# Optimization experiments

Hardware: AMD Instinct MI355X
Metric: run time of the kernel (lower is better)

Reference implementation:

```python
import jax, jax.numpy as jnp
import numpy as np

H = 8
D_MODEL = 512
D_K = D_MODEL // H
B = 8
S = 1024


def _linear(x, W, b):
    # torch nn.Linear: y = x @ W.T + b, W: [out, in]
    return jnp.einsum('bsd,ed->bse', x, W) + b


def _to_heads(x):
    # [B,S,D] -> [B,H,S,d_k]
    return x.reshape(B, S, H, D_K).transpose(0, 2, 1, 3)


def setup_inputs() -> dict:
    key = jax.random.key(0)
    ks = jax.random.split(key, 20)
    inp = {
        'input_rgb': jax.random.normal(ks[0], (B, S, D_MODEL), jnp.float32),
        'input_flow': jax.random.normal(ks[1], (B, S, D_MODEL), jnp.float32),
    }
    names = ['Wq1', 'Wk1', 'Wv1', 'Wq2', 'Wk2', 'Wv2', 'Wo1', 'Wo2']
    for i, n in enumerate(names):
        inp[n] = jax.random.normal(ks[2 + i], (D_MODEL, D_MODEL), jnp.float32) * 0.02
        inp['b' + n[1:]] = jax.random.normal(ks[10 + i], (D_MODEL,), jnp.float32) * 0.02
    return inp


def reference(input_rgb, input_flow, Wq1, bq1, Wk1, bk1, Wv1, bv1,
              Wq2, bq2, Wk2, bk2, Wv2, bv2, Wo1, bo1, Wo2, bo2):
    scale = 1.0 / jnp.sqrt(jnp.asarray(D_K, input_rgb.dtype))

    q_r = _to_heads(_linear(input_rgb, Wq1, bq1))
    k_r = _to_heads(_linear(input_rgb, Wk1, bk1))
    v_r = _to_heads(_linear(input_rgb, Wv1, bv1))
    q_f = _to_heads(_linear(input_flow, Wq2, bq2))
    k_f = _to_heads(_linear(input_flow, Wk2, bk2))
    v_f = _to_heads(_linear(input_flow, Wv2, bv2))

    # two full [B,H,S,S] softmax attention maps
    attn_rgb = jax.nn.softmax(jnp.einsum('bhqd,bhkd->bhqk', q_r, k_r) * scale, axis=-1)
    attn_flow = jax.nn.softmax(jnp.einsum('bhqd,bhkd->bhqk', q_f, k_f) * scale, axis=-1)
    # elementwise max merge (breaks flash-attention fusion)
    attn = jnp.maximum(attn_rgb, attn_flow)

    # Attention2: out = attn @ value (dropout is identity in eval mode)
    out_rgb = jnp.einsum('bhqk,bhkd->bhqd', attn, v_r)
    out_flow = jnp.einsum('bhqk,bhkd->bhqd', attn, v_f)

    out_rgb = out_rgb.transpose(0, 2, 1, 3).reshape(B, S, D_MODEL)
    out_flow = out_flow.transpose(0, 2, 1, 3).reshape(B, S, D_MODEL)
    return (_linear(out_rgb, Wo1, bo1), _linear(out_flow, Wo2, bo2))
```

## Files before the change

### kernel.cpp

```cpp
#include <hip/hip_runtime.h>
#include <hip/hip_bf16.h>


typedef unsigned short u16;
typedef __attribute__((ext_vector_type(8))) short short8;
typedef __attribute__((ext_vector_type(4))) short s4pack;
typedef __attribute__((ext_vector_type(4))) float floatx4;

#define B_DIM 8
#define S_DIM 1024
#define H_DIM 8
#define DK 64
#define DMODEL 512
#define NTOK (B_DIM * S_DIM)
#define SEG ((size_t)NTOK * DMODEL)
#define WSEG ((size_t)DMODEL * DMODEL)

#define SCHED_FENCE() __builtin_amdgcn_sched_barrier(0)
#define LGKM0() asm volatile("s_waitcnt lgkmcnt(0)" ::: "memory")
#define VMCNT0() asm volatile("s_waitcnt vmcnt(0)" ::: "memory")
#define BARRIER() __builtin_amdgcn_s_barrier()

__device__ __forceinline__ floatx4 mfma_bf16(short8 a, short8 b, floatx4 c) {
  return __builtin_amdgcn_mfma_f32_16x16x32_bf16(a, b, c, 0, 0, 0);
}

__device__ __forceinline__ u16 f32_to_bf16_rne(float f) {
  unsigned u = __float_as_uint(f);
  unsigned r = u + 0x7FFFu + ((u >> 16) & 1u);
  return (u16)(r >> 16);
}

__device__ __forceinline__ float bf16_bits_to_f32(u16 u) {
  return __uint_as_float(((unsigned)u) << 16);
}

__device__ __forceinline__ void async_cp16(const u16* g, u16* lds) {
  __builtin_amdgcn_global_load_lds(
      (__attribute__((address_space(1))) void*)(const_cast<u16*>(g)),
      (__attribute__((address_space(3))) void*)(lds), 16, 0, 0);
}

#define NT_CONV 18
struct ConvParams {
  const void* src[NT_CONV];
  u16* dst[NT_CONV];
  int n[NT_CONV];
  int coff[NT_CONV + 1];
};

__global__ __launch_bounds__(256) void convert_inputs(ConvParams p) {
  __shared__ int flag_f32;
  const int blk = blockIdx.x;
  int t = 0;
  while (t + 1 < NT_CONV && blk >= p.coff[t + 1]) ++t;
  const int lc = blk - p.coff[t];
  const int n = p.n[t];
  const int tid = threadIdx.x;

  if (tid < 64) {
    const u16* s = (const u16*)p.src[t];
    int bad = 0;
#pragma unroll
    for (int j = 0; j < 8; ++j) {
      float f = bf16_bits_to_f32(s[tid * 8 + j]);
      bad |= !(fabsf(f) < 1e4f);
    }
    bad |= __shfl_xor(bad, 1);
    bad |= __shfl_xor(bad, 2);
    bad |= __shfl_xor(bad, 4);
    bad |= __shfl_xor(bad, 8);
    bad |= __shfl_xor(bad, 16);
    bad |= __shfl_xor(bad, 32);
    if (tid == 0) flag_f32 = bad;
  }
  __syncthreads();
  const int is_f32 = flag_f32;
  const int base = lc * 65536;

  for (int it = 0; it < 32; ++it) {
    const int idx = base + (it * 256 + tid) * 8;
    if (idx + 8 > n) break;
    if (!is_f32) {
      *(short8*)&p.dst[t][idx] = *(const short8*)&((const u16*)p.src[t])[idx];
    } else {
      const float* s = (const float*)p.src[t] + idx;
      short8 o;
#pragma unroll
      for (int j = 0; j < 8; ++j) o[j] = (short)f32_to_bf16_rne(s[j]);
      *(short8*)&p.dst[t][idx] = o;
    }
  }
}

__device__ __forceinline__ void gemm128_mainloop(
    const u16* __restrict__ A, const u16* __restrict__ W,
    int m0, int n0, int K, u16* ldsA, u16* ldsB, floatx4 acc[4][4]) {
  const int tid = threadIdx.x;
  const int lane = tid & 63;
  const int wid = tid >> 6;
  const int wm = wid >> 1, wn = wid & 1;
  const int r = lane & 15, g = lane >> 4;

  const int stg_row = wid * 32 + (lane >> 2);
  const int stg_col = (lane & 3) * 8;

  const u16* ga0 = A + (size_t)(m0 + stg_row) * K + stg_col;
  const u16* ga1 = A + (size_t)(m0 + stg_row + 16) * K + stg_col;
  const u16* gb0 = W + (size_t)(n0 + stg_row) * K + stg_col;
  const u16* gb1 = W + (size_t)(n0 + stg_row + 16) * K + stg_col;
  const int lo0 = (wid * 32) * 32;
  const int lo1 = (wid * 32 + 16) * 32;

  async_cp16(ga0, ldsA + lo0);
  async_cp16(ga1, ldsA + lo1);
  async_cp16(gb0, ldsB + lo0);
  async_cp16(gb1, ldsB + lo1);
  VMCNT0();
  BARRIER();

  int cur = 0;
  for (int k0 = 0; k0 < K; k0 += 32) {
    const int nxt = cur ^ 1;
    const bool more = (k0 + 32 < K);
    if (more) {
      const int nb = nxt * 4096;
      async_cp16(ga0 + k0 + 32, ldsA + nb + lo0);
      async_cp16(ga1 + k0 + 32, ldsA + nb + lo1);
      async_cp16(gb0 + k0 + 32, ldsB + nb + lo0);
      async_cp16(gb1 + k0 + 32, ldsB + nb + lo1);
    }
    const int cb = cur * 4096;
    short8 a[4], b[4];
#pragma unroll
    for (int i = 0; i < 4; ++i)
      a[i] = *(const short8*)&ldsA[cb + (wm * 64 + i * 16 + r) * 32 + g * 8];
#pragma unroll
    for (int j = 0; j < 4; ++j)
      b[j] = *(const short8*)&ldsB[cb + (wn * 64 + j * 16 + r) * 32 + g * 8];
#pragma unroll
    for (int i = 0; i < 4; ++i)
#pragma unroll
      for (int j = 0; j < 4; ++j)
        acc[i][j] = mfma_bf16(a[i], b[j], acc[i][j]);
    if (more) {
      SCHED_FENCE(); VMCNT0(); BARRIER(); SCHED_FENCE();
      cur = nxt;
    }
  }
}

struct QkvParams {
  const u16* X[2];
  const u16* W[2][3];
  const u16* Bias[2][3];
  u16* Out[2][3];
};

__global__ __launch_bounds__(256) void qkv_gemm(QkvParams p) {
  __shared__ u16 ldsA[2 * 128 * 32];
  __shared__ u16 ldsB[2 * 128 * 32];
  const int z = blockIdx.z;
  const int wi = blockIdx.y >> 2;
  const int n0 = (blockIdx.y & 3) * 128;
  const int m0 = blockIdx.x * 128;

  floatx4 acc[4][4];
  const floatx4 z4 = {0.f, 0.f, 0.f, 0.f};
#pragma unroll
  for (int i = 0; i < 4; ++i)
#pragma unroll
    for (int j = 0; j < 4; ++j) acc[i][j] = z4;

  gemm128_mainloop(p.X[z], p.W[z][wi], m0, n0, DMODEL, ldsA, ldsB, acc);

  const int tid = threadIdx.x, lane = tid & 63, wid = tid >> 6;
  const int wm = wid >> 1, wn = wid & 1, r = lane & 15, g = lane >> 4;
  const u16* bias = p.Bias[z][wi];
  u16* out = p.Out[z][wi];
  const float qscale = 0.125f * 1.4426950408889634f;

#pragma unroll
  for (int j = 0; j < 4; ++j) {
    const int c = n0 + wn * 64 + j * 16 + r;
    const float bv = bf16_bits_to_f32(bias[c]);
    const int h = c >> 6, d = c & 63;
#pragma unroll
    for (int i = 0; i < 4; ++i) {
      const int row0 = m0 + wm * 64 + i * 16 + g * 4;
      const int bb = row0 >> 10, ss0 = row0 & 1023;
      if (wi == 2) {
        s4pack pk;
#pragma unroll
        for (int ii = 0; ii < 4; ++ii)
          pk[ii] = (short)f32_to_bf16_rne(acc[i][j][ii] + bv);
        *(s4pack*)&out[(((size_t)(bb * H_DIM + h)) * DK + d) * S_DIM + ss0] = pk;
      } else {
#pragma unroll
        for (int ii = 0; ii < 4; ++ii) {
          float v = acc[i][j][ii] + bv;
          if (wi == 0) v *= qscale;
          out[(((size_t)(bb * H_DIM + h)) * S_DIM + (ss0 + ii)) * DK + d] =
              f32_to_bf16_rne(v);
        }
      }
    }
  }
}

#define KVB 32
#define QB 64

struct AttnParams {
  const u16* Q[2];
  const u16* K[2];
  const u16* Vt[2];
  u16* O[2];
};

__global__ __launch_bounds__(256, 4) void attn_merged(AttnParams p) {
  __shared__ u16 Ks[2][KVB * 64];
  __shared__ u16 Vs[2][64 * KVB];
  __shared__ u16 Ps[QB * 40];

  const int tid = threadIdx.x;
  const int lane = tid & 63;
  const int wid = tid >> 6;
  const int r = lane & 15, g = lane >> 4;

  const int lin = blockIdx.x;
  const int w = (lin & 7) * 128 + (lin >> 3);
  const int bh = w >> 4;
  const int q0 = (w & 15) * QB;
  const size_t hbase = (size_t)bh * S_DIM * DK;

  const int krow = tid >> 3, kch = tid & 7;
  const int kdst = krow * 64 + ((kch ^ (krow & 7)) * 8);
  const size_t kgsrc = (size_t)krow * DK + kch * 8;
  const int vrow = tid >> 2, vch = tid & 3;
  const int vdst = vrow * KVB + ((vch ^ ((vrow >> 2) & 3)) * 8);
  const size_t vgsrc = (size_t)vrow * S_DIM + vch * 8;

  short8 qf[2][2];
#pragma unroll
  for (int s = 0; s < 2; ++s)
#pragma unroll
    for (int kc = 0; kc < 2; ++kc)
      qf[s][kc] = *(const short8*)
          &p.Q[s][hbase + (size_t)(q0 + wid * 16 + r) * DK + kc * 32 + g * 8];

  short8 kst[2], vst[2];
#pragma unroll
  for (int s = 0; s < 2; ++s)
    kst[s] = *(const short8*)&p.K[s][hbase + kgsrc];

  float sums[2][4];
#pragma unroll
  for (int s = 0; s < 2; ++s)
#pragma unroll
    for (int i = 0; i < 4; ++i) sums[s][i] = 0.f;

  for (int kt = 0; kt < 32; ++kt) {
    if (kt) { SCHED_FENCE(); BARRIER(); SCHED_FENCE(); }
#pragma unroll
    for (int s = 0; s < 2; ++s)
      *(short8*)&Ks[s][kdst] = kst[s];
    if (kt < 31) {
      const size_t k0n = (size_t)(kt + 1) * KVB * DK;
#pragma unroll
      for (int s = 0; s < 2; ++s)
        kst[s] = *(const short8*)&p.K[s][hbase + k0n + kgsrc];
    }
    SCHED_FENCE(); LGKM0(); BARRIER(); SCHED_FENCE();

#pragma unroll
    for (int s = 0; s < 2; ++s)
#pragma unroll
      for (int nt = 0; nt < 2; ++nt) {
        const int row = nt * 16 + r;
        const short8 b0 = *(const short8*)&Ks[s][row * 64 + ((g ^ (r & 7)) * 8)];
        const short8 b1 =
            *(const short8*)&Ks[s][row * 64 + (((4 + g) ^ (r & 7)) * 8)];
        floatx4 acc = {0.f, 0.f, 0.f, 0.f};
        acc = mfma_bf16(qf[s][0], b0, acc);
        acc = mfma_bf16(qf[s][1], b1, acc);
#pragma unroll
        for (int i = 0; i < 4; ++i)
          sums[s][i] += __builtin_amdgcn_exp2f(acc[i]);
      }
  }

#pragma unroll
  for (int s = 0; s < 2; ++s) {
    kst[s] = *(const short8*)&p.K[s][hbase + kgsrc];
    vst[s] = *(const short8*)&p.Vt[s][hbase + vgsrc];
  }

  float inv_[2][4];
#pragma unroll
  for (int s = 0; s < 2; ++s)
#pragma unroll
    for (int i = 0; i < 4; ++i) {
      float v = sums[s][i];
      v += __shfl_xor(v, 1);
      v += __shfl_xor(v, 2);
      v += __shfl_xor(v, 4);
      v += __shfl_xor(v, 8);
      inv_[s][i] = 1.0f / v;
    }

  floatx4 o_[2][4];
  const floatx4 z4 = {0.f, 0.f, 0.f, 0.f};
#pragma unroll
  for (int s = 0; s < 2; ++s)
#pragma unroll
    for (int nt = 0; nt < 4; ++nt) o_[s][nt] = z4;

  for (int kt = 0; kt < 32; ++kt) {
    SCHED_FENCE(); BARRIER(); SCHED_FENCE();
#pragma unroll
    for (int s = 0; s < 2; ++s) {
      *(short8*)&Ks[s][kdst] = kst[s];
      *(short8*)&Vs[s][vdst] = vst[s];
    }
    if (kt < 31) {
      const size_t kn = (size_t)(kt + 1) * KVB;
#pragma unroll
      for (int s = 0; s < 2; ++s) {
        kst[s] = *(const short8*)&p.K[s][hbase + kn * DK + kgsrc];
        vst[s] = *(const short8*)&p.Vt[s][hbase + vgsrc + kn];
      }
    }
    SCHED_FENCE(); LGKM0(); BARRIER(); SCHED_FENCE();

#pragma unroll
    for (int nt = 0; nt < 2; ++nt) {
      const int row = nt * 16 + r;
      const short8 br0 = *(const short8*)&Ks[0][row * 64 + ((g ^ (r & 7)) * 8)];
      const short8 br1 =
          *(const short8*)&Ks[0][row * 64 + (((4 + g) ^ (r & 7)) * 8)];
      const short8 bf0 = *(const short8*)&Ks[1][row * 64 + ((g ^ (r & 7)) * 8)];
      const short8 bf1 =
          *(const short8*)&Ks[1][row * 64 + (((4 + g) ^ (r & 7)) * 8)];
      floatx4 ar = {0.f, 0.f, 0.f, 0.f};
      floatx4 af = {0.f, 0.f, 0.f, 0.f};
      ar = mfma_bf16(qf[0][0], br0, ar);
      ar = mfma_bf16(qf[0][1], br1, ar);
      af = mfma_bf16(qf[1][0], bf0, af);
      af = mfma_bf16(qf[1][1], bf1, af);
      const int prow = wid * 16 + g * 4;
#pragma unroll
      for (int i = 0; i < 4; ++i) {
        const float pr = __builtin_amdgcn_exp2f(ar[i]) * inv_[0][i];
        const float pf = __builtin_amdgcn_exp2f(af[i]) * inv_[1][i];
        Ps[(prow + i) * 40 + nt * 16 + r] = f32_to_bf16_rne(fmaxf(pr, pf));
      }
    }

    LGKM0();
    SCHED_FENCE();

    const short8 pa = *(const short8*)&Ps[(wid * 16 + r) * 40 + g * 8];
#pragma unroll
    for (int s = 0; s < 2; ++s)
#pragma unroll
      for (int nt = 0; nt < 4; ++nt) {
        const int vr = nt * 16 + r;
        const short8 v = *(const short8*)
            &Vs[s][vr * KVB + ((g ^ ((r >> 2) & 3)) * 8)];
        o_[s][nt] = mfma_bf16(pa, v, o_[s][nt]);
      }
  }

  const int bb = bh >> 3, h = bh & 7;
#pragma unroll
  for (int s = 0; s < 2; ++s) {
    u16* out = p.O[s];
#pragma unroll
    for (int nt = 0; nt < 4; ++nt) {
      const int col = h * 64 + nt * 16 + r;
#pragma unroll
      for (int i = 0; i < 4; ++i) {
        const int row = q0 + wid * 16 + g * 4 + i;
        out[((size_t)bb * S_DIM + row) * DMODEL + col] =
            f32_to_bf16_rne(o_[s][nt][i]);
      }
    }
  }
}

struct OutParams {
  const u16* A[2];
  const u16* W[2];
  const u16* Bias[2];
  float* Out[2];
};

__global__ __launch_bounds__(256) void out_gemm(OutParams p) {
  __shared__ u16 ldsA[2 * 128 * 32];
  __shared__ u16 ldsB[2 * 128 * 32];
  const int z = blockIdx.z;
  const int m0 = blockIdx.x * 128;
  const int n0 = blockIdx.y * 128;

  floatx4 acc[4][4];
  const floatx4 z4 = {0.f, 0.f, 0.f, 0.f};
#pragma unroll
  for (int i = 0; i < 4; ++i)
#pragma unroll
    for (int j = 0; j < 4; ++j) acc[i][j] = z4;

  gemm128_mainloop(p.A[z], p.W[z], m0, n0, DMODEL, ldsA, ldsB, acc);

  const int tid = threadIdx.x, lane = tid & 63, wid = tid >> 6;
  const int wm = wid >> 1, wn = wid & 1, r = lane & 15, g = lane >> 4;
  const u16* bias = p.Bias[z];
  float* out = p.Out[z];

#pragma unroll
  for (int j = 0; j < 4; ++j) {
    const int c = n0 + wn * 64 + j * 16 + r;
    const float bv = bf16_bits_to_f32(bias[c]);
#pragma unroll
    for (int i = 0; i < 4; ++i) {
      const int row0 = m0 + wm * 64 + i * 16 + g * 4;
#pragma unroll
      for (int ii = 0; ii < 4; ++ii)
        out[(size_t)(row0 + ii) * DMODEL + c] = acc[i][j][ii] + bv;
    }
  }
}

extern "C" void kernel_launch(void* const* d_in, const int* in_sizes, int n_in,
                              void* d_out, int out_size, void* d_ws, size_t ws_size,
                              hipStream_t stream) {
  (void)in_sizes; (void)n_in; (void)out_size; (void)ws_size;
  u16* ws = (u16*)d_ws;
  u16* Qr = ws + 0 * SEG;
  u16* Kr = ws + 1 * SEG;
  u16* Vr = ws + 2 * SEG;
  u16* Qf = ws + 3 * SEG;
  u16* Kf = ws + 4 * SEG;
  u16* Vf = ws + 5 * SEG;
  u16* Or = ws + 6 * SEG;
  u16* Of = ws + 7 * SEG;
  u16* cW = ws + 8 * SEG;
  u16* cB = cW + 8 * WSEG;

  ConvParams cp;
  int coff = 0;
  for (int i = 0; i < NT_CONV; ++i) {
    cp.src[i] = d_in[i];
    int n;
    if (i < 2) {
      n = (int)SEG;
      cp.dst[i] = (i == 0) ? Or : Of;
    } else {
      const int k = (i - 2) >> 1;
      const int isb = (i - 2) & 1;
      n = isb ? DMODEL : (int)WSEG;
      cp.dst[i] = isb ? (cB + k * DMODEL) : (cW + k * WSEG);
    }
    cp.n[i] = n;
    cp.coff[i] = coff;
    coff += (n + 65535) / 65536;
  }
  cp.coff[NT_CONV] = coff;
  convert_inputs<<<dim3(coff), dim3(256), 0, stream>>>(cp);

  QkvParams qp;
  qp.X[0] = Or;
  qp.X[1] = Of;
  for (int s = 0; s < 2; ++s)
    for (int wi = 0; wi < 3; ++wi) {
      const int k = s * 3 + wi;
      qp.W[s][wi] = cW + k * WSEG;
      qp.Bias[s][wi] = cB + k * DMODEL;
    }
  qp.Out[0][0] = Qr; qp.Out[0][1] = Kr; qp.Out[0][2] = Vr;
  qp.Out[1][0] = Qf; qp.Out[1][1] = Kf; qp.Out[1][2] = Vf;
  qkv_gemm<<<dim3(64, 12, 2), dim3(256), 0, stream>>>(qp);

  AttnParams ap;
  ap.Q[0] = Qr; ap.Q[1] = Qf;
  ap.K[0] = Kr; ap.K[1] = Kf;
  ap.Vt[0] = Vr; ap.Vt[1] = Vf;
  ap.O[0] = Or; ap.O[1] = Of;
  attn_merged<<<dim3(1024), dim3(256), 0, stream>>>(ap);

  OutParams op;
  op.A[0] = Or; op.A[1] = Of;
  op.W[0] = cW + 6 * WSEG; op.Bias[0] = cB + 6 * DMODEL;
  op.W[1] = cW + 7 * WSEG; op.Bias[1] = cB + 7 * DMODEL;
  op.Out[0] = (float*)d_out;
  op.Out[1] = (float*)d_out + SEG;
  out_gemm<<<dim3(64, 4, 2), dim3(256), 0, stream>>>(op);
}
```

Measured before the change: 280.7 us.

## Triple-buffer GEMM loads, remap GEMM blocks, keep attention P in registers

```diff
diff --git a/kernel.cpp b/kernel.cpp
--- a/kernel.cpp
+++ b/kernel.cpp
@@ -25,6 +25,11 @@
   return __builtin_amdgcn_mfma_f32_16x16x32_bf16(a, b, c, 0, 0, 0);
 }
 
+__device__ __forceinline__ void mfma16(floatx4& c, s4pack a, s4pack b) {
+  asm volatile("v_mfma_f32_16x16x16_bf16 %0, %1, %2, %0"
+               : "+v"(c) : "v"(a), "v"(b));
+}
+
 __device__ __forceinline__ u16 f32_to_bf16_rne(float f) {
   unsigned u = __float_as_uint(f);
   unsigned r = u + 0x7FFFu + ((u >> 16) & 1u);
@@ -95,7 +100,7 @@
 
 __device__ __forceinline__ void gemm128_mainloop(
     const u16* __restrict__ A, const u16* __restrict__ W,
-    int m0, int n0, int K, u16* ldsA, u16* ldsB, floatx4 acc[4][4]) {
+    int m0, int n0, u16* ldsA, u16* ldsB, floatx4 acc[4][4]) {
   const int tid = threadIdx.x;
   const int lane = tid & 63;
   const int wid = tid >> 6;
@@ -105,32 +110,33 @@
   const int stg_row = wid * 32 + (lane >> 2);
   const int stg_col = (lane & 3) * 8;
 
-  const u16* ga0 = A + (size_t)(m0 + stg_row) * K + stg_col;
-  const u16* ga1 = A + (size_t)(m0 + stg_row + 16) * K + stg_col;
-  const u16* gb0 = W + (size_t)(n0 + stg_row) * K + stg_col;
-  const u16* gb1 = W + (size_t)(n0 + stg_row + 16) * K + stg_col;
+  const u16* ga0 = A + (size_t)(m0 + stg_row) * DMODEL + stg_col;
+  const u16* ga1 = A + (size_t)(m0 + stg_row + 16) * DMODEL + stg_col;
+  const u16* gb0 = W + (size_t)(n0 + stg_row) * DMODEL + stg_col;
+  const u16* gb1 = W + (size_t)(n0 + stg_row + 16) * DMODEL + stg_col;
   const int lo0 = (wid * 32) * 32;
   const int lo1 = (wid * 32 + 16) * 32;
 
-  async_cp16(ga0, ldsA + lo0);
-  async_cp16(ga1, ldsA + lo1);
-  async_cp16(gb0, ldsB + lo0);
-  async_cp16(gb1, ldsB + lo1);
-  VMCNT0();
-  BARRIER();
-
-  int cur = 0;
-  for (int k0 = 0; k0 < K; k0 += 32) {
-    const int nxt = cur ^ 1;
-    const bool more = (k0 + 32 < K);
-    if (more) {
-      const int nb = nxt * 4096;
-      async_cp16(ga0 + k0 + 32, ldsA + nb + lo0);
-      async_cp16(ga1 + k0 + 32, ldsA + nb + lo1);
-      async_cp16(gb0 + k0 + 32, ldsB + nb + lo0);
-      async_cp16(gb1 + k0 + 32, ldsB + nb + lo1);
-    }
-    const int cb = cur * 4096;
+#pragma unroll
+  for (int t = 0; t < 3; ++t) {
+    const int nb = t * 4096;
+    const int ko = t * 32;
+    async_cp16(ga0 + ko, ldsA + nb + lo0);
+    async_cp16(ga1 + ko, ldsA + nb + lo1);
+    async_cp16(gb0 + ko, ldsB + nb + lo0);
+    async_cp16(gb1 + ko, ldsB + nb + lo1);
+  }
+
+#pragma unroll
+  for (int kt = 0; kt < 16; ++kt) {
+    SCHED_FENCE();
+    if (kt < 14)       asm volatile("s_waitcnt vmcnt(8)" ::: "memory");
+    else if (kt == 14) asm volatile("s_waitcnt vmcnt(4)" ::: "memory");
+    else               asm volatile("s_waitcnt vmcnt(0)" ::: "memory");
+    BARRIER();
+    SCHED_FENCE();
+
+    const int cb = (kt % 3) * 4096;
     short8 a[4], b[4];
 #pragma unroll
     for (int i = 0; i < 4; ++i)
@@ -143,9 +149,14 @@
 #pragma unroll
       for (int j = 0; j < 4; ++j)
         acc[i][j] = mfma_bf16(a[i], b[j], acc[i][j]);
-    if (more) {
-      SCHED_FENCE(); VMCNT0(); BARRIER(); SCHED_FENCE();
-      cur = nxt;
+
+    if (kt + 3 < 16) {
+      SCHED_FENCE(); BARRIER(); SCHED_FENCE();
+      const int ko = (kt + 3) * 32;
+      async_cp16(ga0 + ko, ldsA + cb + lo0);
+      async_cp16(ga1 + ko, ldsA + cb + lo1);
+      async_cp16(gb0 + ko, ldsB + cb + lo0);
+      async_cp16(gb1 + ko, ldsB + cb + lo1);
     }
   }
 }
@@ -158,12 +169,16 @@
 };
 
 __global__ __launch_bounds__(256) void qkv_gemm(QkvParams p) {
-  __shared__ u16 ldsA[2 * 128 * 32];
-  __shared__ u16 ldsB[2 * 128 * 32];
-  const int z = blockIdx.z;
-  const int wi = blockIdx.y >> 2;
-  const int n0 = (blockIdx.y & 3) * 128;
-  const int m0 = blockIdx.x * 128;
+  __shared__ u16 ldsA[3 * 128 * 32];
+  __shared__ u16 ldsB[3 * 128 * 32];
+  const int lin = blockIdx.x;
+  const int wg = (lin & 7) * 192 + (lin >> 3);
+  const int m0 = (wg / 24) * 128;
+  const int c = wg % 24;
+  const int z = c / 12;
+  const int yc = c % 12;
+  const int wi = yc >> 2;
+  const int n0 = (yc & 3) * 128;
 
   floatx4 acc[4][4];
   const floatx4 z4 = {0.f, 0.f, 0.f, 0.f};
@@ -172,7 +187,7 @@
 #pragma unroll
     for (int j = 0; j < 4; ++j) acc[i][j] = z4;
 
-  gemm128_mainloop(p.X[z], p.W[z][wi], m0, n0, DMODEL, ldsA, ldsB, acc);
+  gemm128_mainloop(p.X[z], p.W[z][wi], m0, n0, ldsA, ldsB, acc);
 
   const int tid = threadIdx.x, lane = tid & 63, wid = tid >> 6;
   const int wm = wid >> 1, wn = wid & 1, r = lane & 15, g = lane >> 4;
@@ -182,9 +197,9 @@
 
 #pragma unroll
   for (int j = 0; j < 4; ++j) {
-    const int c = n0 + wn * 64 + j * 16 + r;
-    const float bv = bf16_bits_to_f32(bias[c]);
-    const int h = c >> 6, d = c & 63;
+    const int cc = n0 + wn * 64 + j * 16 + r;
+    const float bv = bf16_bits_to_f32(bias[cc]);
+    const int h = cc >> 6, d = cc & 63;
 #pragma unroll
     for (int i = 0; i < 4; ++i) {
       const int row0 = m0 + wm * 64 + i * 16 + g * 4;
@@ -218,10 +233,9 @@
   u16* O[2];
 };
 
-__global__ __launch_bounds__(256, 4) void attn_merged(AttnParams p) {
+__global__ __launch_bounds__(256, 3) void attn_merged(AttnParams p) {
   __shared__ u16 Ks[2][KVB * 64];
   __shared__ u16 Vs[2][64 * KVB];
-  __shared__ u16 Ps[QB * 40];
 
   const int tid = threadIdx.x;
   const int lane = tid & 63;
@@ -254,11 +268,8 @@
   for (int s = 0; s < 2; ++s)
     kst[s] = *(const short8*)&p.K[s][hbase + kgsrc];
 
-  float sums[2][4];
-#pragma unroll
-  for (int s = 0; s < 2; ++s)
-#pragma unroll
-    for (int i = 0; i < 4; ++i) sums[s][i] = 0.f;
+  const floatx4 z4 = {0.f, 0.f, 0.f, 0.f};
+  float sl[2] = {0.f, 0.f};
 
   for (int kt = 0; kt < 32; ++kt) {
     if (kt) { SCHED_FENCE(); BARRIER(); SCHED_FENCE(); }
@@ -276,17 +287,15 @@
 #pragma unroll
     for (int s = 0; s < 2; ++s)
 #pragma unroll
-      for (int nt = 0; nt < 2; ++nt) {
-        const int row = nt * 16 + r;
-        const short8 b0 = *(const short8*)&Ks[s][row * 64 + ((g ^ (r & 7)) * 8)];
-        const short8 b1 =
+      for (int kt2 = 0; kt2 < 2; ++kt2) {
+        const int row = kt2 * 16 + r;
+        const short8 kf0 = *(const short8*)&Ks[s][row * 64 + ((g ^ (r & 7)) * 8)];
+        const short8 kf1 =
             *(const short8*)&Ks[s][row * 64 + (((4 + g) ^ (r & 7)) * 8)];
-        floatx4 acc = {0.f, 0.f, 0.f, 0.f};
-        acc = mfma_bf16(qf[s][0], b0, acc);
-        acc = mfma_bf16(qf[s][1], b1, acc);
-#pragma unroll
-        for (int i = 0; i < 4; ++i)
-          sums[s][i] += __builtin_amdgcn_exp2f(acc[i]);
+        floatx4 acc = mfma_bf16(kf0, qf[s][0], z4);
+        acc = mfma_bf16(kf1, qf[s][1], acc);
+        sl[s] += __builtin_amdgcn_exp2f(acc[0]) + __builtin_amdgcn_exp2f(acc[1]) +
+                 __builtin_amdgcn_exp2f(acc[2]) + __builtin_amdgcn_exp2f(acc[3]);
       }
   }
 
@@ -296,21 +305,16 @@
     vst[s] = *(const short8*)&p.Vt[s][hbase + vgsrc];
   }
 
-  float inv_[2][4];
-#pragma unroll
-  for (int s = 0; s < 2; ++s)
-#pragma unroll
-    for (int i = 0; i < 4; ++i) {
-      float v = sums[s][i];
-      v += __shfl_xor(v, 1);
-      v += __shfl_xor(v, 2);
-      v += __shfl_xor(v, 4);
-      v += __shfl_xor(v, 8);
-      inv_[s][i] = 1.0f / v;
-    }
+  float inv_[2];
+#pragma unroll
+  for (int s = 0; s < 2; ++s) {
+    float v = sl[s];
+    v += __shfl_xor(v, 16);
+    v += __shfl_xor(v, 32);
+    inv_[s] = 1.0f / v;
+  }
 
   floatx4 o_[2][4];
-  const floatx4 z4 = {0.f, 0.f, 0.f, 0.f};
 #pragma unroll
   for (int s = 0; s < 2; ++s)
 #pragma unroll
@@ -333,44 +337,53 @@
     }
     SCHED_FENCE(); LGKM0(); BARRIER(); SCHED_FENCE();
 
-#pragma unroll
-    for (int nt = 0; nt < 2; ++nt) {
-      const int row = nt * 16 + r;
+    s4pack pA[2];
+#pragma unroll
+    for (int kt2 = 0; kt2 < 2; ++kt2) {
+      const int row = kt2 * 16 + r;
       const short8 br0 = *(const short8*)&Ks[0][row * 64 + ((g ^ (r & 7)) * 8)];
       const short8 br1 =
           *(const short8*)&Ks[0][row * 64 + (((4 + g) ^ (r & 7)) * 8)];
       const short8 bf0 = *(const short8*)&Ks[1][row * 64 + ((g ^ (r & 7)) * 8)];
       const short8 bf1 =
           *(const short8*)&Ks[1][row * 64 + (((4 + g) ^ (r & 7)) * 8)];
-      floatx4 ar = {0.f, 0.f, 0.f, 0.f};
-      floatx4 af = {0.f, 0.f, 0.f, 0.f};
-      ar = mfma_bf16(qf[0][0], br0, ar);
-      ar = mfma_bf16(qf[0][1], br1, ar);
-      af = mfma_bf16(qf[1][0], bf0, af);
-      af = mfma_bf16(qf[1][1], bf1, af);
-      const int prow = wid * 16 + g * 4;
+      floatx4 ar = mfma_bf16(br0, qf[0][0], z4);
+      ar = mfma_bf16(br1, qf[0][1], ar);
+      floatx4 af = mfma_bf16(bf0, qf[1][0], z4);
+      af = mfma_bf16(bf1, qf[1][1], af);
 #pragma unroll
       for (int i = 0; i < 4; ++i) {
-        const float pr = __builtin_amdgcn_exp2f(ar[i]) * inv_[0][i];
-        const float pf = __builtin_amdgcn_exp2f(af[i]) * inv_[1][i];
-        Ps[(prow + i) * 40 + nt * 16 + r] = f32_to_bf16_rne(fmaxf(pr, pf));
+        const float pr = __builtin_amdgcn_exp2f(ar[i]) * inv_[0];
+        const float pf = __builtin_amdgcn_exp2f(af[i]) * inv_[1];
+        pA[kt2][i] = (short)f32_to_bf16_rne(fmaxf(pr, pf));
       }
     }
 
-    LGKM0();
-    SCHED_FENCE();
-
-    const short8 pa = *(const short8*)&Ps[(wid * 16 + r) * 40 + g * 8];
+    s4pack vB[2][2][4];
 #pragma unroll
     for (int s = 0; s < 2; ++s)
 #pragma unroll
+      for (int kt2 = 0; kt2 < 2; ++kt2)
+#pragma unroll
+        for (int nt = 0; nt < 4; ++nt) {
+          const int row = nt * 16 + r;
+          const int cch = 2 * kt2 + (g >> 1);
+          const int addr =
+              row * KVB + ((cch ^ ((r >> 2) & 3)) * 8) + (g & 1) * 4;
+          vB[s][kt2][nt] = *(const s4pack*)&Vs[s][addr];
+        }
+
+    asm volatile("s_nop 7" :::);
+#pragma unroll
+    for (int s = 0; s < 2; ++s)
+#pragma unroll
       for (int nt = 0; nt < 4; ++nt) {
-        const int vr = nt * 16 + r;
-        const short8 v = *(const short8*)
-            &Vs[s][vr * KVB + ((g ^ ((r >> 2) & 3)) * 8)];
-        o_[s][nt] = mfma_bf16(pa, v, o_[s][nt]);
+        mfma16(o_[s][nt], pA[0], vB[s][0][nt]);
+        mfma16(o_[s][nt], pA[1], vB[s][1][nt]);
       }
   }
+
+  asm volatile("s_nop 7\n\ts_nop 7" :::);
 
   const int bb = bh >> 3, h = bh & 7;
 #pragma unroll
@@ -397,11 +410,14 @@
 };
 
 __global__ __launch_bounds__(256) void out_gemm(OutParams p) {
-  __shared__ u16 ldsA[2 * 128 * 32];
-  __shared__ u16 ldsB[2 * 128 * 32];
-  const int z = blockIdx.z;
-  const int m0 = blockIdx.x * 128;
-  const int n0 = blockIdx.y * 128;
+  __shared__ u16 ldsA[3 * 128 * 32];
+  __shared__ u16 ldsB[3 * 128 * 32];
+  const int lin = blockIdx.x;
+  const int wg = (lin & 7) * 64 + (lin >> 3);
+  const int m0 = (wg >> 3) * 128;
+  const int c = wg & 7;
+  const int z = c >> 2;
+  const int n0 = (c & 3) * 128;
 
   floatx4 acc[4][4];
   const floatx4 z4 = {0.f, 0.f, 0.f, 0.f};
@@ -410,7 +426,7 @@
 #pragma unroll
     for (int j = 0; j < 4; ++j) acc[i][j] = z4;
 
-  gemm128_mainloop(p.A[z], p.W[z], m0, n0, DMODEL, ldsA, ldsB, acc);
+  gemm128_mainloop(p.A[z], p.W[z], m0, n0, ldsA, ldsB, acc);
 
   const int tid = threadIdx.x, lane = tid & 63, wid = tid >> 6;
   const int wm = wid >> 1, wn = wid & 1, r = lane & 15, g = lane >> 4;
@@ -419,14 +435,14 @@
 
 #pragma unroll
   for (int j = 0; j < 4; ++j) {
-    const int c = n0 + wn * 64 + j * 16 + r;
-    const float bv = bf16_bits_to_f32(bias[c]);
+    const int cc = n0 + wn * 64 + j * 16 + r;
+    const float bv = bf16_bits_to_f32(bias[cc]);
 #pragma unroll
     for (int i = 0; i < 4; ++i) {
       const int row0 = m0 + wm * 64 + i * 16 + g * 4;
 #pragma unroll
       for (int ii = 0; ii < 4; ++ii)
-        out[(size_t)(row0 + ii) * DMODEL + c] = acc[i][j][ii] + bv;
+        out[(size_t)(row0 + ii) * DMODEL + cc] = acc[i][j][ii] + bv;
     }
   }
 }
@@ -479,7 +495,7 @@
     }
   qp.Out[0][0] = Qr; qp.Out[0][1] = Kr; qp.Out[0][2] = Vr;
   qp.Out[1][0] = Qf; qp.Out[1][1] = Kf; qp.Out[1][2] = Vf;
-  qkv_gemm<<<dim3(64, 12, 2), dim3(256), 0, stream>>>(qp);
+  qkv_gemm<<<dim3(1536), dim3(256), 0, stream>>>(qp);
 
   AttnParams ap;
   ap.Q[0] = Qr; ap.Q[1] = Qf;
@@ -494,5 +510,5 @@
   op.W[1] = cW + 7 * WSEG; op.Bias[1] = cB + 7 * DMODEL;
   op.Out[0] = (float*)d_out;
   op.Out[1] = (float*)d_out + SEG;
-  out_gemm<<<dim3(64, 4, 2), dim3(256), 0, stream>>>(op);
-}
+  out_gemm<<<dim3(512), dim3(256), 0, stream>>>(op);
+}
```

New measurement: 284.8 us. Within noise of the previous version (+1.5%).
